# Kernel optimization log

Measured on AMD Instinct MI355X. Metric: run time of the kernel, lower is better.

Reference implementation:

```python
import jax, jax.numpy as jnp
import numpy as np

B, L = 2, 1024
D_MODEL, N_LAYER = 768, 2
D_INNER, D_STATE, D_CONV, DT_RANK = 1536, 16, 4, 48
D_INT, VOCAB = 1536, 32000
EPS = 1e-5


def layernorm(x, w, b):
    m = x.mean(-1, keepdims=True)
    v = ((x - m) ** 2).mean(-1, keepdims=True)
    return (x - m) * jax.lax.rsqrt(v + EPS) * w + b


def silu(x):
    return x * jax.nn.sigmoid(x)


def depthwise_causal_conv(x, w, b):
    # x: (B,L,D); w: (D,K) torch depthwise weight squeezed; b: (D,)
    k = w.shape[-1]
    kern = w.T[:, None, :]  # (K,1,D) for 'WIO' with feature_group_count=D
    y = jax.lax.conv_general_dilated(
        x, kern, window_strides=(1,), padding=[(k - 1, 0)],
        dimension_numbers=('NWC', 'WIO', 'NWC'),
        feature_group_count=x.shape[-1])
    return y + b


def selective_scan(u, delta, A, Bm, Cm, Dp):
    # u, delta: (B,L,Dn); A: (Dn,N); Bm, Cm: (B,L,N); Dp: (Dn,)
    dA = jnp.exp(delta[..., None] * A)                         # (B,L,Dn,N)
    dBu = delta[..., None] * Bm[:, :, None, :] * u[..., None]  # (B,L,Dn,N)

    def step(h, inp):
        dA_t, dBu_t, C_t = inp
        h = dA_t * h + dBu_t
        return h, jnp.einsum('bdn,bn->bd', h, C_t)

    h0 = jnp.zeros((u.shape[0], A.shape[0], A.shape[1]), u.dtype)
    _, ys = jax.lax.scan(step, h0, (jnp.swapaxes(dA, 0, 1), jnp.swapaxes(dBu, 0, 1), jnp.swapaxes(Cm, 0, 1)))
    return jnp.swapaxes(ys, 0, 1) + u * Dp


def mamba_mixer(x, p):
    xz = x @ p['in_proj'].T                     # (B,L,2*Dn)
    xin, z = jnp.split(xz, 2, axis=-1)
    xc = silu(depthwise_causal_conv(xin, p['conv_w'], p['conv_b']))
    x_dbl = xc @ p['x_proj'].T                  # (B,L,dt_rank+2N)
    dt, Bm, Cm = jnp.split(x_dbl, [DT_RANK, DT_RANK + D_STATE], axis=-1)
    delta = jax.nn.softplus(dt @ p['dt_w'].T + p['dt_b'])
    A = -jnp.exp(p['A_log'])
    y = selective_scan(xc, delta, A, Bm, Cm, p['D'])
    y = y * silu(z)
    return y @ p['out_proj'].T


def block(h, res, p):
    # mamba_ssm Block (non-fused path) with GatedMLP
    res = h + res if res is not None else h
    x = layernorm(res, p['norm_w'], p['norm_b'])
    x = mamba_mixer(x, p)
    res = x + res
    x = layernorm(res, p['norm2_w'], p['norm2_b'])
    y, gate = jnp.split(x @ p['fc1'].T, 2, axis=-1)
    x = (y * silu(gate)) @ p['fc2'].T
    return x, res


def _forward(input_ids, embed, norm_w, norm_b, in_proj, conv_w, conv_b, x_proj,
             dt_w, dt_b, A_log, D, out_proj, norm2_w, norm2_b, fc1, fc2,
             normf_w, normf_b):
    h = embed[input_ids]
    res = None
    for i in range(N_LAYER):
        p = dict(norm_w=norm_w[i], norm_b=norm_b[i], in_proj=in_proj[i],
                 conv_w=conv_w[i], conv_b=conv_b[i], x_proj=x_proj[i],
                 dt_w=dt_w[i], dt_b=dt_b[i], A_log=A_log[i], D=D[i],
                 out_proj=out_proj[i], norm2_w=norm2_w[i], norm2_b=norm2_b[i],
                 fc1=fc1[i], fc2=fc2[i])
        h_f, r_f = block(h, res, p)
        h_f = layernorm(h_f, normf_w, normf_b)
        res_flip = res[:, ::-1] if res is not None else None
        h_b, r_b = block(h[:, ::-1], res_flip, p)
        h_b = layernorm(h_b, normf_w, normf_b)
        h = h_f + h_b[:, ::-1]
        res = r_f + r_b[:, ::-1]
    # dropout is identity at inference
    res = h + res
    h = layernorm(res, normf_w, normf_b)
    return h.mean(axis=1)  # (B, d_model)


def setup_inputs() -> dict:
    key = jax.random.key(0)
    ks = iter(jax.random.split(key, 32))

    def rn(shape, scale=0.02):
        return jax.random.normal(next(ks), shape, jnp.float32) * scale

    inp = {}
    inp['input_ids'] = jax.random.randint(next(ks), (B, L), 0, VOCAB)
    inp['embed'] = rn((VOCAB, D_MODEL))
    inp['norm_w'] = jnp.ones((N_LAYER, D_MODEL), jnp.float32)
    inp['norm_b'] = jnp.zeros((N_LAYER, D_MODEL), jnp.float32)
    inp['in_proj'] = rn((N_LAYER, 2 * D_INNER, D_MODEL))
    inp['conv_w'] = rn((N_LAYER, D_INNER, D_CONV), 0.2)
    inp['conv_b'] = jnp.zeros((N_LAYER, D_INNER), jnp.float32)
    inp['x_proj'] = rn((N_LAYER, DT_RANK + 2 * D_STATE, D_INNER))
    inp['dt_w'] = rn((N_LAYER, D_INNER, DT_RANK), 0.1)
    # inverse-softplus of ~0.01 so delta starts small (matches mamba dt init spirit)
    inp['dt_b'] = jnp.full((N_LAYER, D_INNER), float(np.log(np.expm1(0.01))), jnp.float32)
    # S4D-real init: A = -(1..d_state)
    inp['A_log'] = jnp.broadcast_to(jnp.log(jnp.arange(1, D_STATE + 1, dtype=jnp.float32)), (N_LAYER, D_INNER, D_STATE)).copy()
    inp['D'] = jnp.ones((N_LAYER, D_INNER), jnp.float32)
    inp['out_proj'] = rn((N_LAYER, D_MODEL, D_INNER))
    inp['norm2_w'] = jnp.ones((N_LAYER, D_MODEL), jnp.float32)
    inp['norm2_b'] = jnp.zeros((N_LAYER, D_MODEL), jnp.float32)
    inp['fc1'] = rn((N_LAYER, 2 * D_INT, D_MODEL))
    inp['fc2'] = rn((N_LAYER, D_MODEL, D_INT))
    inp['normf_w'] = jnp.ones((D_MODEL,), jnp.float32)
    inp['normf_b'] = jnp.zeros((D_MODEL,), jnp.float32)
    return inp


def reference(input_ids, embed, norm_w, norm_b, in_proj, conv_w, conv_b, x_proj,
              dt_w, dt_b, A_log, D, out_proj, norm2_w, norm2_b, fc1, fc2,
              normf_w, normf_b):
    return _forward(input_ids, embed, norm_w, norm_b, in_proj, conv_w, conv_b,
                    x_proj, dt_w, dt_b, A_log, D, out_proj, norm2_w, norm2_b,
                    fc1, fc2, normf_w, normf_b)
```

## Files before the change

kernel.cpp:

```cpp
#include <hip/hip_runtime.h>
#include <cstddef>

#define BB 2
#define LL 1024
#define DM 768
#define DI 1536
#define NST 16
#define DTR 48
#define DINT 1536
#define NLAYER 2
#define ML (BB*LL)
#define NCH 32
#define CLEN (LL/NCH)

typedef __attribute__((ext_vector_type(8))) short s16x8;
typedef __attribute__((ext_vector_type(4))) float f32x4;

typedef __attribute__((address_space(1))) void* gas_t;
typedef __attribute__((address_space(3))) void* las_t;

static __device__ __forceinline__ float sigm(float x){ return 1.f/(1.f+__expf(-x)); }
static __device__ __forceinline__ float silu_(float x){ return x*sigm(x); }
static __device__ __forceinline__ float softplus_(float x){ return fmaxf(x,0.f)+log1pf(__expf(-fabsf(x))); }
static __device__ __forceinline__ unsigned short f2b(float x){
  unsigned int u = __float_as_uint(x);
  unsigned int r = (u + 0x7fffu + ((u>>16)&1u)) >> 16;
  return (unsigned short)r;
}
static __device__ __forceinline__ float b2f(unsigned short v){
  return __uint_as_float(((unsigned int)v) << 16);
}

__global__ void k_embed(const int* __restrict__ ids, const float* __restrict__ emb,
                        float* __restrict__ out){
  int idx = blockIdx.x*256 + threadIdx.x;
  if (idx >= ML*DM) return;
  int c = idx % DM; int bl = idx / DM;
  out[idx] = emb[(size_t)ids[bl]*DM + c];
}

struct Seg8 { const float* src[8]; unsigned short* dst[8]; int cum[9]; };
__global__ void k_f2bseg(Seg8 p){
  int idx = blockIdx.x*256 + threadIdx.x;
  if (idx >= p.cum[8]) return;
  int s = 0;
  #pragma unroll
  for (int i = 1; i < 8; i++) s += (idx >= p.cum[i]);
  int local = idx - p.cum[s];
  p.dst[s][local] = f2b(p.src[s][local]);
}

__global__ void k_wbig(const float* __restrict__ dw, const float* __restrict__ xp,
                       unsigned short* __restrict__ wb){
  int idx = blockIdx.x*256 + threadIdx.x;
  if (idx >= 1664*DI) return;
  int j = idx % DI, i = idx / DI;
  unsigned short v;
  if (i < DI){
    float s = 0.f;
    #pragma unroll
    for (int k = 0; k < DTR; k++) s += dw[i*DTR + k] * xp[(size_t)k*DI + j];
    v = f2b(s);
  } else {
    int r = i - DI;
    v = (r < 32) ? f2b(xp[(size_t)(DTR + r)*DI + j]) : (unsigned short)0;
  }
  wb[idx] = v;
}

__global__ __launch_bounds__(256) void k_ln(const float* __restrict__ x,
    const float* __restrict__ add, const float* __restrict__ w, const float* __restrict__ bi,
    float* __restrict__ sumout, float* __restrict__ fout, unsigned short* __restrict__ bout,
    int rows){
  int wv = threadIdx.x >> 6, lane = threadIdx.x & 63;
  int row = blockIdx.x*4 + wv;
  if (row >= rows) return;
  const float* xr = x + (size_t)row*DM;
  float v[12]; float s = 0.f, sq = 0.f;
  #pragma unroll
  for (int i = 0; i < 12; i++){
    int c = lane + 64*i;
    float t = xr[c];
    if (add) t += add[(size_t)row*DM + c];
    if (sumout) sumout[(size_t)row*DM + c] = t;
    v[i] = t; s += t; sq += t*t;
  }
  #pragma unroll
  for (int o = 32; o; o >>= 1){ s += __shfl_xor(s, o, 64); sq += __shfl_xor(sq, o, 64); }
  float mean = s*(1.f/DM);
  float var  = sq*(1.f/DM) - mean*mean;
  float rstd = rsqrtf(var + 1e-5f);
  #pragma unroll
  for (int i = 0; i < 12; i++){
    int c = lane + 64*i;
    float o = (v[i]-mean)*rstd*w[c] + bi[c];
    if (fout) fout[(size_t)row*DM + c] = o;
    if (bout) bout[(size_t)row*DM + c] = f2b(o);
  }
}

__global__ __launch_bounds__(256) void k_lnfin(const float* __restrict__ mlpo,
    const float* __restrict__ resd, const float* __restrict__ w, const float* __restrict__ bi,
    float* __restrict__ h, float* __restrict__ res){
  int wv = threadIdx.x >> 6, lane = threadIdx.x & 63;
  int row = blockIdx.x*4 + wv;
  if (row >= ML) return;
  const float* x0 = mlpo + (size_t)row*DM;
  const float* x1 = mlpo + (size_t)(ML + row)*DM;
  float v0[12], v1[12]; float s0=0,q0=0,s1=0,q1=0;
  #pragma unroll
  for (int i = 0; i < 12; i++){
    int c = lane + 64*i;
    float a = x0[c], b = x1[c];
    v0[i]=a; v1[i]=b; s0+=a; q0+=a*a; s1+=b; q1+=b*b;
  }
  #pragma unroll
  for (int o = 32; o; o >>= 1){
    s0 += __shfl_xor(s0, o, 64); q0 += __shfl_xor(q0, o, 64);
    s1 += __shfl_xor(s1, o, 64); q1 += __shfl_xor(q1, o, 64);
  }
  float m0 = s0*(1.f/DM), m1 = s1*(1.f/DM);
  float r0 = rsqrtf(q0*(1.f/DM) - m0*m0 + 1e-5f);
  float r1 = rsqrtf(q1*(1.f/DM) - m1*m1 + 1e-5f);
  #pragma unroll
  for (int i = 0; i < 12; i++){
    int c = lane + 64*i;
    float o = ((v0[i]-m0)*r0 + (v1[i]-m1)*r1)*w[c] + 2.f*bi[c];
    h[(size_t)row*DM + c] = o;
    res[(size_t)row*DM + c] = resd[(size_t)row*DM + c] + resd[(size_t)(ML+row)*DM + c];
  }
}

static __device__ __forceinline__ void tile_mn(int &mT, int &nT){
  int nx = gridDim.x;
  int orig = blockIdx.y * nx + blockIdx.x;
  int nwg = nx * gridDim.y;
  int q = nwg >> 3, r = nwg & 7;
  int xcd = orig & 7, j = orig >> 3;
  int wg = (xcd < r ? xcd*(q+1) : r*(q+1) + (xcd-r)*q) + j;
  mT = wg / nx; nT = wg - mT*nx;
}

static __device__ __forceinline__ void mgemm_core(
    const unsigned short* __restrict__ A, const unsigned short* __restrict__ W, int K,
    int m0, int n0,
    unsigned short* As, unsigned short* Bs, f32x4 (&acc)[4][2]){
  int t = threadIdx.x;
  int lane = t & 63, w = t >> 6;
  int wm = w & 1, wn = w >> 1;

  const unsigned short* gA[4]; unsigned short* lA[4];
  #pragma unroll
  for (int si = 0; si < 4; si++){
    int s = t + si*256;
    int kk = s >> 9, s2 = s & 511;
    int row = ((s2>>6)<<4) + (s2 & 15);
    int ko  = (((s2>>4) & 3) << 3) + kk*32;
    gA[si] = A + (size_t)(m0+row)*K + ko;
    lA[si] = As + (size_t)s*8;
  }
  const unsigned short* gB[2]; unsigned short* lB[2];
  #pragma unroll
  for (int si = 0; si < 2; si++){
    int s = t + si*256;
    int kk = s >> 8, s2 = s & 255;
    int row = ((s2>>6)<<4) + (s2 & 15);
    int ko  = (((s2>>4) & 3) << 3) + kk*32;
    gB[si] = W + (size_t)(n0+row)*K + ko;
    lB[si] = Bs + (size_t)s*8;
  }

  #pragma unroll
  for (int si = 0; si < 4; si++)
    __builtin_amdgcn_global_load_lds((gas_t)gA[si], (las_t)lA[si], 16, 0, 0);
  #pragma unroll
  for (int si = 0; si < 2; si++)
    __builtin_amdgcn_global_load_lds((gas_t)gB[si], (las_t)lB[si], 16, 0, 0);

  int NI = K >> 6;
  int cur = 0;
  for (int it = 0; it < NI; ++it){
    if (it + 1 < NI){
      int kn = (it+1) << 6, nb = cur ^ 1;
      #pragma unroll
      for (int si = 0; si < 4; si++)
        __builtin_amdgcn_global_load_lds((gas_t)(gA[si] + kn), (las_t)(lA[si] + nb*8192), 16, 0, 0);
      #pragma unroll
      for (int si = 0; si < 2; si++)
        __builtin_amdgcn_global_load_lds((gas_t)(gB[si] + kn), (las_t)(lB[si] + nb*4096), 16, 0, 0);
      asm volatile("s_waitcnt vmcnt(6)" ::: "memory");
    } else {
      asm volatile("s_waitcnt vmcnt(0)" ::: "memory");
    }
    __builtin_amdgcn_s_barrier();
    __builtin_amdgcn_sched_barrier(0);
    const unsigned short* Ab = As + cur*8192;
    const unsigned short* Bb = Bs + cur*4096;
    #pragma unroll
    for (int kk = 0; kk < 2; kk++){
      s16x8 af[4], bf[2];
      #pragma unroll
      for (int i = 0; i < 4; i++) af[i] = *(const s16x8*)&Ab[kk*4096 + ((wm*4+i)*64 + lane)*8];
      #pragma unroll
      for (int j = 0; j < 2; j++) bf[j] = *(const s16x8*)&Bb[kk*2048 + ((wn*2+j)*64 + lane)*8];
      #pragma unroll
      for (int i = 0; i < 4; i++)
        #pragma unroll
        for (int j = 0; j < 2; j++)
          acc[i][j] = __builtin_amdgcn_mfma_f32_16x16x32_bf16(af[i], bf[j], acc[i][j], 0, 0, 0);
    }
    __builtin_amdgcn_s_barrier();
    __builtin_amdgcn_sched_barrier(0);
    cur ^= 1;
  }
}

__global__ __launch_bounds__(256) void k_mg0(const unsigned short* __restrict__ A,
    const unsigned short* __restrict__ W, const float* __restrict__ addsrc,
    float* __restrict__ Cf, int N, int K){
  __shared__ __align__(16) unsigned short As[16384], Bs[8192];
  int mT, nT; tile_mn(mT, nT);
  int m0 = mT*128, n0 = nT*64;
  f32x4 acc[4][2] = {};
  mgemm_core(A, W, K, m0, n0, As, Bs, acc);
  int t = threadIdx.x, lane = t & 63, w = t >> 6;
  int wm = w & 1, wn = w >> 1;
  int cl = lane & 15, qd = lane >> 4;
  #pragma unroll
  for (int i = 0; i < 4; i++){
    int mbase = m0 + (wm*4+i)*16 + qd*4;
    #pragma unroll
    for (int j = 0; j < 2; j++){
      int n = n0 + (wn*2+j)*16 + cl;
      #pragma unroll
      for (int r = 0; r < 4; r++){
        int m = mbase + r;
        float v = acc[i][j][r];
        if (addsrc) v += addsrc[(size_t)(m & (ML-1))*N + n];
        Cf[(size_t)m*N + n] = v;
      }
    }
  }
}

__global__ __launch_bounds__(256) void k_mg1(const unsigned short* __restrict__ A,
    const unsigned short* __restrict__ W, const float* __restrict__ dtb,
    unsigned short* __restrict__ dlb, float* __restrict__ bcout, int K){
  __shared__ __align__(16) unsigned short As[16384], Bs[8192];
  int mT, nT; tile_mn(mT, nT);
  int m0 = mT*128, n0 = nT*64;
  f32x4 acc[4][2] = {};
  mgemm_core(A, W, K, m0, n0, As, Bs, acc);
  int t = threadIdx.x, lane = t & 63, w = t >> 6;
  int wm = w & 1, wn = w >> 1;
  int cl = lane & 15, qd = lane >> 4;
  #pragma unroll
  for (int i = 0; i < 4; i++){
    int mbase = m0 + (wm*4+i)*16 + qd*4;
    #pragma unroll
    for (int j = 0; j < 2; j++){
      int n = n0 + (wn*2+j)*16 + cl;
      #pragma unroll
      for (int r = 0; r < 4; r++){
        int m = mbase + r;
        float v = acc[i][j][r];
        if (n < DI) dlb[(size_t)m*DI + n] = f2b(softplus_(v + dtb[n]));
        else if (n < DI + 32) bcout[(size_t)m*32 + (n - DI)] = v;
      }
    }
  }
}

__global__ __launch_bounds__(256) void k_mg2(const unsigned short* __restrict__ A,
    const unsigned short* __restrict__ W, unsigned short* __restrict__ Cb, int N, int K){
  __shared__ __align__(16) unsigned short As[16384], Bs[8192];
  int mT, nT; tile_mn(mT, nT);
  int m0 = mT*128, n0 = nT*64;
  f32x4 acc[4][2] = {};
  mgemm_core(A, W, K, m0, n0, As, Bs, acc);
  int t = threadIdx.x, lane = t & 63, w = t >> 6;
  int wm = w & 1, wn = w >> 1;
  int cl = lane & 15, qd = lane >> 4;
  #pragma unroll
  for (int i = 0; i < 4; i++){
    int mbase = m0 + (wm*4+i)*16 + qd*4;
    #pragma unroll
    for (int j = 0; j < 2; j++){
      int n = n0 + (wn*2+j)*16 + cl;
      #pragma unroll
      for (int r = 0; r < 4; r++){
        int m = mbase + r;
        Cb[(size_t)m*N + n] = f2b(acc[i][j][r]);
      }
    }
  }
}

__global__ void k_conv(const unsigned short* __restrict__ xzb, const float* __restrict__ w,
                       const float* __restrict__ bi, unsigned short* __restrict__ xcb){
  int idx = blockIdx.x*256 + threadIdx.x;
  if (idx >= 2*ML*DI) return;
  int d = idx % DI; int r = idx / DI;
  int bl = r % ML; int dir = r / ML;
  int t = bl % LL; int b = bl / LL;
  float acc = bi[d];
  #pragma unroll
  for (int k = 0; k < 4; k++){
    int tp = dir ? (t + 3 - k) : (t - 3 + k);
    if (tp >= 0 && tp < LL)
      acc += w[d*4 + k] * b2f(xzb[((size_t)(b*LL + tp))*(2*DI) + d]);
  }
  xcb[idx] = f2b(silu_(acc));
}

__global__ __launch_bounds__(256) void k_scan1(
    const unsigned short* __restrict__ dlb, const unsigned short* __restrict__ xcb,
    const float* __restrict__ bc, const float* __restrict__ A_log,
    float* __restrict__ sA, float* __restrict__ sH){
  __shared__ float Bsh[CLEN*16];
  int blk = blockIdx.x;
  int dgrp = blk % (DI/256); int rest = blk / (DI/256);
  int ch = rest % NCH; rest /= NCH;
  int b = rest & 1; int dir = rest >> 1;
  int d = dgrp*256 + threadIdx.x;
  int t0 = dir ? (LL-1 - ch*CLEN) : ch*CLEN;
  long step = dir ? -1 : 1;
  long row0 = (long)dir*ML + b*LL + t0;
  #pragma unroll
  for (int rep = 0; rep < CLEN*16/256; rep++){
    int e = threadIdx.x + rep*256;
    int s = e >> 4, n = e & 15;
    Bsh[e] = bc[(size_t)(row0 + s*step)*32 + n];
  }
  __syncthreads();
  float ea[16];
  #pragma unroll
  for (int n = 0; n < 16; n++) ea[n] = -__expf(A_log[d*16 + n]) * 1.44269504f;
  float h[16], P[16];
  #pragma unroll
  for (int n = 0; n < 16; n++){ h[n] = 0.f; P[n] = 1.f; }
  long row = row0;
  for (int s = 0; s < CLEN; s++){
    float de = b2f(dlb[(size_t)row*DI + d]);
    float u  = b2f(xcb[(size_t)row*DI + d]);
    float duu = de*u;
    float Ba[16];
    const f32x4* Bv = (const f32x4*)&Bsh[s*16];
    *(f32x4*)&Ba[0] = Bv[0]; *(f32x4*)&Ba[4] = Bv[1];
    *(f32x4*)&Ba[8] = Bv[2]; *(f32x4*)&Ba[12] = Bv[3];
    #pragma unroll
    for (int n = 0; n < 16; n++){
      float dA = exp2f(de*ea[n]);
      h[n] = dA*h[n] + duu*Ba[n];
      P[n] *= dA;
    }
    row += step;
  }
  size_t sbase = ((((size_t)dir*BB + b)*NCH + ch)*DI + d)*16;
  #pragma unroll
  for (int n = 0; n < 16; n++){ sA[sbase+n] = P[n]; sH[sbase+n] = h[n]; }
}

__global__ __launch_bounds__(256) void k_prefix(
    float* __restrict__ sA, const float* __restrict__ sH){
  int gid = blockIdx.x*256 + threadIdx.x;
  int dn = gid % (DI*16);
  int db_ = gid / (DI*16);
  float h = 0.f;
  size_t base = (size_t)db_*NCH*DI*16 + dn;
  for (int ch = 0; ch < NCH; ch++){
    size_t idx = base + (size_t)ch*DI*16;
    float a = sA[idx], hh = sH[idx];
    sA[idx] = h;
    h = hh + a*h;
  }
}

__global__ __launch_bounds__(256) void k_scan2(
    const unsigned short* __restrict__ dlb, const unsigned short* __restrict__ xcb,
    const float* __restrict__ bc, const unsigned short* __restrict__ xzb,
    const float* __restrict__ A_log, const float* __restrict__ Dp,
    const float* __restrict__ h0, unsigned short* __restrict__ y){
  __shared__ float BCs[CLEN*32];
  int blk = blockIdx.x;
  int dgrp = blk % (DI/256); int rest = blk / (DI/256);
  int ch = rest % NCH; rest /= NCH;
  int b = rest & 1; int dir = rest >> 1;
  int d = dgrp*256 + threadIdx.x;
  int t0 = dir ? (LL-1 - ch*CLEN) : ch*CLEN;
  long step = dir ? -1 : 1;
  long row0 = (long)dir*ML + b*LL + t0;
  #pragma unroll
  for (int rep = 0; rep < CLEN*32/256; rep++){
    int e = threadIdx.x + rep*256;
    int s = e >> 5, n = e & 31;
    BCs[e] = bc[(size_t)(row0 + s*step)*32 + n];
  }
  __syncthreads();
  float ea[16];
  #pragma unroll
  for (int n = 0; n < 16; n++) ea[n] = -__expf(A_log[d*16 + n]) * 1.44269504f;
  float dD = Dp[d];
  float h[16];
  size_t hbase = ((((size_t)dir*BB + b)*NCH + ch)*DI + d)*16;
  #pragma unroll
  for (int n = 0; n < 16; n++) h[n] = h0[hbase + n];
  long row = row0;
  long zoff = (long)dir*ML;
  for (int s = 0; s < CLEN; s++){
    float de = b2f(dlb[(size_t)row*DI + d]);
    float u  = b2f(xcb[(size_t)row*DI + d]);
    float z  = b2f(xzb[(size_t)(row - zoff)*(2*DI) + DI + d]);
    float duu = de*u;
    float Ba[16], Ca[16];
    const f32x4* Bv = (const f32x4*)&BCs[s*32];
    *(f32x4*)&Ba[0] = Bv[0]; *(f32x4*)&Ba[4] = Bv[1];
    *(f32x4*)&Ba[8] = Bv[2]; *(f32x4*)&Ba[12] = Bv[3];
    *(f32x4*)&Ca[0] = Bv[4]; *(f32x4*)&Ca[4] = Bv[5];
    *(f32x4*)&Ca[8] = Bv[6]; *(f32x4*)&Ca[12] = Bv[7];
    float p0 = 0.f, p1 = 0.f, p2 = 0.f, p3 = 0.f;
    #pragma unroll
    for (int n = 0; n < 16; n += 4){
      float dA0 = exp2f(de*ea[n]),   dA1 = exp2f(de*ea[n+1]);
      float dA2 = exp2f(de*ea[n+2]), dA3 = exp2f(de*ea[n+3]);
      h[n]   = dA0*h[n]   + duu*Ba[n];
      h[n+1] = dA1*h[n+1] + duu*Ba[n+1];
      h[n+2] = dA2*h[n+2] + duu*Ba[n+2];
      h[n+3] = dA3*h[n+3] + duu*Ba[n+3];
      p0 = fmaf(h[n],   Ca[n],   p0);
      p1 = fmaf(h[n+1], Ca[n+1], p1);
      p2 = fmaf(h[n+2], Ca[n+2], p2);
      p3 = fmaf(h[n+3], Ca[n+3], p3);
    }
    float p = (p0+p1) + (p2+p3);
    y[(size_t)row*DI + d] = f2b((p + u*dD) * silu_(z));
    row += step;
  }
}

__global__ void k_gate(const unsigned short* __restrict__ fc1o, unsigned short* __restrict__ g){
  int idx = blockIdx.x*256 + threadIdx.x;
  if (idx >= 2*ML*DINT) return;
  int i = idx % DINT; int bl = idx / DINT;
  float aa = b2f(fc1o[(size_t)bl*2*DINT + i]);
  float gt = b2f(fc1o[(size_t)bl*2*DINT + DINT + i]);
  g[idx] = f2b(aa * silu_(gt));
}

__global__ void k_mean(const float* __restrict__ x, float* __restrict__ out){
  int d = blockIdx.x*256 + threadIdx.x;
  int b = blockIdx.y;
  if (d >= DM) return;
  float s = 0.f;
  for (int t = 0; t < LL; t++) s += x[((size_t)(b*LL + t))*DM + d];
  out[b*DM + d] = s*(1.f/LL);
}

extern "C" void kernel_launch(void* const* d_in, const int* in_sizes, int n_in,
                              void* d_out, int out_size, void* d_ws, size_t ws_size,
                              hipStream_t stream){
  const int*   ids     = (const int*)d_in[0];
  const float* embed   = (const float*)d_in[1];
  const float* norm_w  = (const float*)d_in[2];
  const float* norm_b  = (const float*)d_in[3];
  const float* in_proj = (const float*)d_in[4];
  const float* conv_w  = (const float*)d_in[5];
  const float* conv_b  = (const float*)d_in[6];
  const float* x_proj  = (const float*)d_in[7];
  const float* dt_w    = (const float*)d_in[8];
  const float* dt_b    = (const float*)d_in[9];
  const float* A_log   = (const float*)d_in[10];
  const float* Dp      = (const float*)d_in[11];
  const float* out_pj  = (const float*)d_in[12];
  const float* norm2_w = (const float*)d_in[13];
  const float* norm2_b = (const float*)d_in[14];
  const float* fc1     = (const float*)d_in[15];
  const float* fc2     = (const float*)d_in[16];
  const float* normf_w = (const float*)d_in[17];
  const float* normf_b = (const float*)d_in[18];
  float* out = (float*)d_out;

  const size_t BLD   = (size_t)ML*DM;
  const size_t BLDI  = (size_t)ML*DI;
  const size_t SUMN  = (size_t)2*BB*NCH*DI*16;

  float* f = (float*)d_ws; size_t off = 0;
  float* h     = f+off; off += BLD;
  float* res   = f+off; off += BLD;
  float* rc    = f+off; off += BLD;
  float* resd  = f+off; off += 2*BLD;
  float* bc    = f+off; off += (size_t)2*ML*32;
  float* sA    = f+off; off += SUMN;
  float* sH    = f+off; off += SUMN;
  unsigned short* gb = (unsigned short*)sH;
  unsigned short* u16 = (unsigned short*)(f + off); size_t uo = 0;
  unsigned short* xlnb = u16+uo; uo += BLD;
  unsigned short* x2b  = u16+uo; uo += 2*BLD;
  unsigned short* xzb  = u16+uo; uo += 2*BLDI;
  unsigned short* xcb  = u16+uo; uo += 2*BLDI;
  unsigned short* dlb  = u16+uo; uo += 2*BLDI;
  unsigned short* wts  = u16+uo;
  const size_t W_IP = (size_t)2*DI*DM, W_OP = (size_t)DM*DI, W_F1 = (size_t)2*DINT*DM,
               W_F2 = (size_t)DM*DINT, W_BG = (size_t)1664*DI;
  const size_t WLAY = W_IP + W_OP + W_F1 + W_F2 + W_BG;
  unsigned short* yb   = xcb;
  unsigned short* fc1o = xcb;
  float*          mlpo = (float*)xcb;
  (void)ws_size; (void)in_sizes; (void)n_in; (void)out_size;

  dim3 blk(256);
  auto cdiv = [](int a, int b){ return (a + b - 1)/b; };
  const int scan_blocks = 2*2*NCH*(DI/256);

  Seg8 sg; int cum = 0;
  for (int l = 0; l < 2; l++){
    unsigned short* wl = wts + (size_t)l*WLAY;
    sg.src[l*4+0] = in_proj + (size_t)l*W_IP; sg.dst[l*4+0] = wl;
    sg.src[l*4+1] = out_pj  + (size_t)l*W_OP; sg.dst[l*4+1] = wl + W_IP;
    sg.src[l*4+2] = fc1     + (size_t)l*W_F1; sg.dst[l*4+2] = wl + W_IP + W_OP;
    sg.src[l*4+3] = fc2     + (size_t)l*W_F2; sg.dst[l*4+3] = wl + W_IP + W_OP + W_F1;
  }
  { int sz[8] = {(int)W_IP,(int)W_OP,(int)W_F1,(int)W_F2,(int)W_IP,(int)W_OP,(int)W_F1,(int)W_F2};
    sg.cum[0]=0; for (int i = 0; i < 8; i++){ cum += sz[i]; sg.cum[i+1] = cum; } }
  k_f2bseg<<<cdiv(cum,256), blk, 0, stream>>>(sg);
  for (int l = 0; l < 2; l++)
    k_wbig<<<cdiv(1664*DI,256), blk, 0, stream>>>(dt_w + (size_t)l*DI*DTR,
        x_proj + (size_t)l*(DTR+2*NST)*DI, wts + (size_t)l*WLAY + W_IP + W_OP + W_F1 + W_F2);

  k_embed<<<cdiv(ML*DM,256), blk, 0, stream>>>(ids, embed, h);

  for (int l = 0; l < NLAYER; l++){
    unsigned short* wl   = wts + (size_t)l*WLAY;
    unsigned short* wib  = wl;
    unsigned short* wob  = wl + W_IP;
    unsigned short* wf1b = wl + W_IP + W_OP;
    unsigned short* wf2b = wl + W_IP + W_OP + W_F1;
    unsigned short* wbig = wl + W_IP + W_OP + W_F1 + W_F2;
    const float* nw  = norm_w  + l*DM;
    const float* nb  = norm_b  + l*DM;
    const float* cw  = conv_w  + (size_t)l*DI*4;
    const float* cb  = conv_b  + (size_t)l*DI;
    const float* db  = dt_b    + (size_t)l*DI;
    const float* al  = A_log   + (size_t)l*DI*NST;
    const float* dpl = Dp      + (size_t)l*DI;
    const float* n2w = norm2_w + l*DM;
    const float* n2b = norm2_b + l*DM;

    k_ln<<<ML/4, blk, 0, stream>>>(h, (l==0)?nullptr:res, nw, nb, rc, nullptr, xlnb, ML);
    k_mg2<<<dim3(2*DI/64, ML/128), blk, 0, stream>>>(xlnb, wib, xzb, 2*DI, DM);
    k_conv<<<cdiv(2*ML*DI,256), blk, 0, stream>>>(xzb, cw, cb, xcb);
    k_mg1<<<dim3(1664/64, 2*ML/128), blk, 0, stream>>>(xcb, wbig, db, dlb, bc, DI);
    k_scan1<<<scan_blocks, blk, 0, stream>>>(dlb, xcb, bc, al, sA, sH);
    k_prefix<<<(2*BB*DI*16)/256, blk, 0, stream>>>(sA, sH);
    k_scan2<<<scan_blocks, blk, 0, stream>>>(dlb, xcb, bc, xzb, al, dpl, sA, yb);
    k_mg0<<<dim3(DM/64, 2*ML/128), blk, 0, stream>>>(yb, wob, rc, resd, DM, DI);
    k_ln<<<2*ML/4, blk, 0, stream>>>(resd, nullptr, n2w, n2b, nullptr, nullptr, x2b, 2*ML);
    k_mg2<<<dim3(2*DINT/64, 2*ML/128), blk, 0, stream>>>(x2b, wf1b, fc1o, 2*DINT, DM);
    k_gate<<<cdiv(2*ML*DINT,256), blk, 0, stream>>>(fc1o, gb);
    k_mg0<<<dim3(DM/64, 2*ML/128), blk, 0, stream>>>(gb, wf2b, nullptr, mlpo, DM, DINT);
    k_lnfin<<<ML/4, blk, 0, stream>>>(mlpo, resd, normf_w, normf_b, h, res);
  }

  k_ln<<<ML/4, blk, 0, stream>>>(h, res, normf_w, normf_b, nullptr, rc, nullptr, ML);
  k_mean<<<dim3(3, BB), blk, 0, stream>>>(rc, out);
}
```

Before: 1.225 ms.

## Template GEMM core on N tile, widen N tiles, halve K step, parallelize mean

The bf16 MFMA GEMM core becomes a template on the N tile width and now steps K by 32 instead of 64, which halves the LDS staging buffers. The in_proj, fc1 and x_proj/dt GEMMs switch to 128x128 tiles for more reuse of each A and B fragment, while the out_proj and fc2 GEMMs keep 128x64 with smaller LDS. The final mean kernel splits the sequence across four wave groups and reduces through shared memory, launching more blocks. The risks are twice as many barriers per K, fewer workgroups for the wider-tile GEMMs, and higher register pressure from the larger accumulators.

Measured after the change: 1.097 ms. 1.12x faster.

```diff
diff --git a/kernel.cpp b/kernel.cpp
--- a/kernel.cpp
+++ b/kernel.cpp
@@ -141,74 +141,75 @@
   mT = wg / nx; nT = wg - mT*nx;
 }
 
+template<int TN>
 static __device__ __forceinline__ void mgemm_core(
     const unsigned short* __restrict__ A, const unsigned short* __restrict__ W, int K,
     int m0, int n0,
-    unsigned short* As, unsigned short* Bs, f32x4 (&acc)[4][2]){
+    unsigned short* As, unsigned short* Bs, f32x4 (&acc)[4][TN/32]){
+  const int NB = TN/32;
+  const int NBS = TN/64;
+  const int ABUF = 4096;
+  const int BBUFS = TN*32;
   int t = threadIdx.x;
   int lane = t & 63, w = t >> 6;
   int wm = w & 1, wn = w >> 1;
 
-  const unsigned short* gA[4]; unsigned short* lA[4];
-  #pragma unroll
-  for (int si = 0; si < 4; si++){
+  const unsigned short* gA[2]; unsigned short* lA[2];
+  #pragma unroll
+  for (int si = 0; si < 2; si++){
     int s = t + si*256;
-    int kk = s >> 9, s2 = s & 511;
-    int row = ((s2>>6)<<4) + (s2 & 15);
-    int ko  = (((s2>>4) & 3) << 3) + kk*32;
+    int row = ((s>>6)<<4) + (s & 15);
+    int ko  = ((s>>4) & 3) << 3;
     gA[si] = A + (size_t)(m0+row)*K + ko;
     lA[si] = As + (size_t)s*8;
   }
   const unsigned short* gB[2]; unsigned short* lB[2];
   #pragma unroll
-  for (int si = 0; si < 2; si++){
+  for (int si = 0; si < NBS; si++){
     int s = t + si*256;
-    int kk = s >> 8, s2 = s & 255;
-    int row = ((s2>>6)<<4) + (s2 & 15);
-    int ko  = (((s2>>4) & 3) << 3) + kk*32;
+    int row = ((s>>6)<<4) + (s & 15);
+    int ko  = ((s>>4) & 3) << 3;
     gB[si] = W + (size_t)(n0+row)*K + ko;
     lB[si] = Bs + (size_t)s*8;
   }
 
   #pragma unroll
-  for (int si = 0; si < 4; si++)
+  for (int si = 0; si < 2; si++)
     __builtin_amdgcn_global_load_lds((gas_t)gA[si], (las_t)lA[si], 16, 0, 0);
   #pragma unroll
-  for (int si = 0; si < 2; si++)
+  for (int si = 0; si < NBS; si++)
     __builtin_amdgcn_global_load_lds((gas_t)gB[si], (las_t)lB[si], 16, 0, 0);
 
-  int NI = K >> 6;
+  int NI = K >> 5;
   int cur = 0;
   for (int it = 0; it < NI; ++it){
     if (it + 1 < NI){
-      int kn = (it+1) << 6, nb = cur ^ 1;
-      #pragma unroll
-      for (int si = 0; si < 4; si++)
-        __builtin_amdgcn_global_load_lds((gas_t)(gA[si] + kn), (las_t)(lA[si] + nb*8192), 16, 0, 0);
+      int kn = (it+1) << 5, nb = cur ^ 1;
       #pragma unroll
       for (int si = 0; si < 2; si++)
-        __builtin_amdgcn_global_load_lds((gas_t)(gB[si] + kn), (las_t)(lB[si] + nb*4096), 16, 0, 0);
-      asm volatile("s_waitcnt vmcnt(6)" ::: "memory");
+        __builtin_amdgcn_global_load_lds((gas_t)(gA[si] + kn), (las_t)(lA[si] + nb*ABUF), 16, 0, 0);
+      #pragma unroll
+      for (int si = 0; si < NBS; si++)
+        __builtin_amdgcn_global_load_lds((gas_t)(gB[si] + kn), (las_t)(lB[si] + nb*BBUFS), 16, 0, 0);
+      if (TN == 128) asm volatile("s_waitcnt vmcnt(4)" ::: "memory");
+      else           asm volatile("s_waitcnt vmcnt(3)" ::: "memory");
     } else {
       asm volatile("s_waitcnt vmcnt(0)" ::: "memory");
     }
     __builtin_amdgcn_s_barrier();
     __builtin_amdgcn_sched_barrier(0);
-    const unsigned short* Ab = As + cur*8192;
-    const unsigned short* Bb = Bs + cur*4096;
-    #pragma unroll
-    for (int kk = 0; kk < 2; kk++){
-      s16x8 af[4], bf[2];
+    const unsigned short* Ab = As + cur*ABUF;
+    const unsigned short* Bb = Bs + cur*BBUFS;
+    s16x8 af[4], bf[NB];
+    #pragma unroll
+    for (int i = 0; i < 4; i++) af[i] = *(const s16x8*)&Ab[((wm*4+i)*64 + lane)*8];
+    #pragma unroll
+    for (int j = 0; j < NB; j++) bf[j] = *(const s16x8*)&Bb[((wn*NB+j)*64 + lane)*8];
+    #pragma unroll
+    for (int i = 0; i < 4; i++)
       #pragma unroll
-      for (int i = 0; i < 4; i++) af[i] = *(const s16x8*)&Ab[kk*4096 + ((wm*4+i)*64 + lane)*8];
-      #pragma unroll
-      for (int j = 0; j < 2; j++) bf[j] = *(const s16x8*)&Bb[kk*2048 + ((wn*2+j)*64 + lane)*8];
-      #pragma unroll
-      for (int i = 0; i < 4; i++)
-        #pragma unroll
-        for (int j = 0; j < 2; j++)
-          acc[i][j] = __builtin_amdgcn_mfma_f32_16x16x32_bf16(af[i], bf[j], acc[i][j], 0, 0, 0);
-    }
+      for (int j = 0; j < NB; j++)
+        acc[i][j] = __builtin_amdgcn_mfma_f32_16x16x32_bf16(af[i], bf[j], acc[i][j], 0, 0, 0);
     __builtin_amdgcn_s_barrier();
     __builtin_amdgcn_sched_barrier(0);
     cur ^= 1;
@@ -218,11 +219,11 @@
 __global__ __launch_bounds__(256) void k_mg0(const unsigned short* __restrict__ A,
     const unsigned short* __restrict__ W, const float* __restrict__ addsrc,
     float* __restrict__ Cf, int N, int K){
-  __shared__ __align__(16) unsigned short As[16384], Bs[8192];
+  __shared__ __align__(16) unsigned short As[8192], Bs[4096];
   int mT, nT; tile_mn(mT, nT);
   int m0 = mT*128, n0 = nT*64;
   f32x4 acc[4][2] = {};
-  mgemm_core(A, W, K, m0, n0, As, Bs, acc);
+  mgemm_core<64>(A, W, K, m0, n0, As, Bs, acc);
   int t = threadIdx.x, lane = t & 63, w = t >> 6;
   int wm = w & 1, wn = w >> 1;
   int cl = lane & 15, qd = lane >> 4;
@@ -246,11 +247,11 @@
 __global__ __launch_bounds__(256) void k_mg1(const unsigned short* __restrict__ A,
     const unsigned short* __restrict__ W, const float* __restrict__ dtb,
     unsigned short* __restrict__ dlb, float* __restrict__ bcout, int K){
-  __shared__ __align__(16) unsigned short As[16384], Bs[8192];
+  __shared__ __align__(16) unsigned short As[8192], Bs[8192];
   int mT, nT; tile_mn(mT, nT);
-  int m0 = mT*128, n0 = nT*64;
-  f32x4 acc[4][2] = {};
-  mgemm_core(A, W, K, m0, n0, As, Bs, acc);
+  int m0 = mT*128, n0 = nT*128;
+  f32x4 acc[4][4] = {};
+  mgemm_core<128>(A, W, K, m0, n0, As, Bs, acc);
   int t = threadIdx.x, lane = t & 63, w = t >> 6;
   int wm = w & 1, wn = w >> 1;
   int cl = lane & 15, qd = lane >> 4;
@@ -258,8 +259,8 @@
   for (int i = 0; i < 4; i++){
     int mbase = m0 + (wm*4+i)*16 + qd*4;
     #pragma unroll
-    for (int j = 0; j < 2; j++){
-      int n = n0 + (wn*2+j)*16 + cl;
+    for (int j = 0; j < 4; j++){
+      int n = n0 + (wn*4+j)*16 + cl;
       #pragma unroll
       for (int r = 0; r < 4; r++){
         int m = mbase + r;
@@ -273,11 +274,11 @@
 
 __global__ __launch_bounds__(256) void k_mg2(const unsigned short* __restrict__ A,
     const unsigned short* __restrict__ W, unsigned short* __restrict__ Cb, int N, int K){
-  __shared__ __align__(16) unsigned short As[16384], Bs[8192];
+  __shared__ __align__(16) unsigned short As[8192], Bs[8192];
   int mT, nT; tile_mn(mT, nT);
-  int m0 = mT*128, n0 = nT*64;
-  f32x4 acc[4][2] = {};
-  mgemm_core(A, W, K, m0, n0, As, Bs, acc);
+  int m0 = mT*128, n0 = nT*128;
+  f32x4 acc[4][4] = {};
+  mgemm_core<128>(A, W, K, m0, n0, As, Bs, acc);
   int t = threadIdx.x, lane = t & 63, w = t >> 6;
   int wm = w & 1, wn = w >> 1;
   int cl = lane & 15, qd = lane >> 4;
@@ -285,8 +286,8 @@
   for (int i = 0; i < 4; i++){
     int mbase = m0 + (wm*4+i)*16 + qd*4;
     #pragma unroll
-    for (int j = 0; j < 2; j++){
-      int n = n0 + (wn*2+j)*16 + cl;
+    for (int j = 0; j < 4; j++){
+      int n = n0 + (wn*4+j)*16 + cl;
       #pragma unroll
       for (int r = 0; r < 4; r++){
         int m = mbase + r;
@@ -447,13 +448,18 @@
   g[idx] = f2b(aa * silu_(gt));
 }
 
-__global__ void k_mean(const float* __restrict__ x, float* __restrict__ out){
-  int d = blockIdx.x*256 + threadIdx.x;
+__global__ __launch_bounds__(256) void k_mean(const float* __restrict__ x, float* __restrict__ out){
+  __shared__ float red[4][64];
+  int dd = threadIdx.x & 63, part = threadIdx.x >> 6;
+  int d = blockIdx.x*64 + dd;
   int b = blockIdx.y;
-  if (d >= DM) return;
   float s = 0.f;
-  for (int t = 0; t < LL; t++) s += x[((size_t)(b*LL + t))*DM + d];
-  out[b*DM + d] = s*(1.f/LL);
+  int tb = part*256;
+  for (int t = tb; t < tb + 256; t++) s += x[((size_t)(b*LL + t))*DM + d];
+  red[part][dd] = s;
+  __syncthreads();
+  if (part == 0)
+    out[b*DM + d] = (red[0][dd]+red[1][dd]+red[2][dd]+red[3][dd])*(1.f/LL);
 }
 
 extern "C" void kernel_launch(void* const* d_in, const int* in_sizes, int n_in,
@@ -547,20 +553,20 @@
     const float* n2b = norm2_b + l*DM;
 
     k_ln<<<ML/4, blk, 0, stream>>>(h, (l==0)?nullptr:res, nw, nb, rc, nullptr, xlnb, ML);
-    k_mg2<<<dim3(2*DI/64, ML/128), blk, 0, stream>>>(xlnb, wib, xzb, 2*DI, DM);
+    k_mg2<<<dim3(2*DI/128, ML/128), blk, 0, stream>>>(xlnb, wib, xzb, 2*DI, DM);
     k_conv<<<cdiv(2*ML*DI,256), blk, 0, stream>>>(xzb, cw, cb, xcb);
-    k_mg1<<<dim3(1664/64, 2*ML/128), blk, 0, stream>>>(xcb, wbig, db, dlb, bc, DI);
+    k_mg1<<<dim3(1664/128, 2*ML/128), blk, 0, stream>>>(xcb, wbig, db, dlb, bc, DI);
     k_scan1<<<scan_blocks, blk, 0, stream>>>(dlb, xcb, bc, al, sA, sH);
     k_prefix<<<(2*BB*DI*16)/256, blk, 0, stream>>>(sA, sH);
     k_scan2<<<scan_blocks, blk, 0, stream>>>(dlb, xcb, bc, xzb, al, dpl, sA, yb);
     k_mg0<<<dim3(DM/64, 2*ML/128), blk, 0, stream>>>(yb, wob, rc, resd, DM, DI);
     k_ln<<<2*ML/4, blk, 0, stream>>>(resd, nullptr, n2w, n2b, nullptr, nullptr, x2b, 2*ML);
-    k_mg2<<<dim3(2*DINT/64, 2*ML/128), blk, 0, stream>>>(x2b, wf1b, fc1o, 2*DINT, DM);
+    k_mg2<<<dim3(2*DINT/128, 2*ML/128), blk, 0, stream>>>(x2b, wf1b, fc1o, 2*DINT, DM);
     k_gate<<<cdiv(2*ML*DINT,256), blk, 0, stream>>>(fc1o, gb);
     k_mg0<<<dim3(DM/64, 2*ML/128), blk, 0, stream>>>(gb, wf2b, nullptr, mlpo, DM, DINT);
     k_lnfin<<<ML/4, blk, 0, stream>>>(mlpo, resd, normf_w, normf_b, h, res);
   }
 
   k_ln<<<ML/4, blk, 0, stream>>>(h, res, normf_w, normf_b, nullptr, rc, nullptr, ML);
-  k_mean<<<dim3(3, BB), blk, 0, stream>>>(rc, out);
-}
+  k_mean<<<dim3(DM/64, BB), blk, 0, stream>>>(rc, out);
+}
```
